# Kernel optimization log

Hardware: AMD Instinct MI355X
Metric: run time of the kernel (lower is better)

The kernel has to match this reference:

```python
import jax, jax.numpy as jnp
import numpy as np

B, C, H, W = 4, 64, 256, 256
HEADS = 8
EPS = 1e-12  # torch F.normalize eps


def _conv(x, w, groups=1, pad='VALID'):
    # x: [B,C,H,W], w: [O, I/groups, kh, kw]
    return jax.lax.conv_general_dilated(
        x, w, window_strides=(1, 1), padding=pad,
        feature_group_count=groups,
        dimension_numbers=('NCHW', 'OIHW', 'NCHW'))


def setup_inputs() -> dict:
    key = jax.random.key(0)
    ks = jax.random.split(key, 8)
    s = 0.02
    return {
        'input1': jax.random.normal(ks[0], (B, C, H, W), jnp.float32),
        'input2': jax.random.normal(ks[1], (B, C, H, W), jnp.float32),
        'q_w': jax.random.normal(ks[2], (C, C, 1, 1), jnp.float32) * s,
        'q_dw_w': jax.random.normal(ks[3], (C, 1, 3, 3), jnp.float32) * s,
        'kv_w': jax.random.normal(ks[4], (2 * C, C, 1, 1), jnp.float32) * s,
        'kv_dw_w': jax.random.normal(ks[5], (2 * C, 1, 3, 3), jnp.float32) * s,
        'proj_w': jax.random.normal(ks[6], (C, C, 1, 1), jnp.float32) * s,
        'temperature': jnp.ones((HEADS, 1, 1), jnp.float32),
    }


def reference(input1, input2, q_w, q_dw_w, kv_w, kv_dw_w, proj_w, temperature):
    b, c, h, w = input1.shape
    hd = c // HEADS  # per-head channels

    q = _conv(_conv(input1, q_w), q_dw_w, groups=c, pad=[(1, 1), (1, 1)])
    kv = _conv(_conv(input2, kv_w), kv_dw_w, groups=2 * c, pad=[(1, 1), (1, 1)])
    k, v = jnp.split(kv, 2, axis=1)

    # b (head c) h w -> b head c (h w)
    def to_heads(t):
        return t.reshape(b, HEADS, hd, h * w)

    q, k, v = to_heads(q), to_heads(k), to_heads(v)

    # L2-normalize over the large hw axis (torch F.normalize semantics)
    q = q / jnp.maximum(jnp.linalg.norm(q, axis=-1, keepdims=True), EPS)
    k = k / jnp.maximum(jnp.linalg.norm(k, axis=-1, keepdims=True), EPS)

    # tiny [b, head, c', c'] channel-attention matrix, contracted over hw
    attn = jnp.einsum('bhcn,bhdn->bhcd', q, k) * temperature
    attn = jax.nn.softmax(attn, axis=-1)
    out = jnp.einsum('bhcd,bhdn->bhcn', attn, v)

    out = out.reshape(b, c, h, w)
    return _conv(out, proj_w)
```

## Files before the change

### kernel.cpp

```cpp
#include <hip/hip_runtime.h>


#define HWN 65536
typedef unsigned short u16;

__device__ __forceinline__ float bf2f(u16 u) {
    return __uint_as_float(((unsigned int)u) << 16);
}
__device__ __forceinline__ u16 f2bf(float f) {
    unsigned int x = __float_as_uint(f);
    x += 0x7FFFu + ((x >> 16) & 1u);
    return (u16)(x >> 16);
}

template<int OC, bool IN_BF16, bool OUT_BF16, bool W_OIC, bool W_PERB>
__global__ __launch_bounds__(256) void pw_gemm(const void* __restrict__ in_v,
                                               const float* __restrict__ w_g,
                                               void* __restrict__ out_v)
{
    constexpr int G = OC / 16;
    constexpr int T = 256 / G;
    constexpr int PXB = T * 4;
    constexpr int NCHUNK = HWN / PXB;
    __shared__ float wlds[64 * OC];

    const int tid = threadIdx.x;
    const int b = blockIdx.y;
    const float* wsrc = w_g + (W_PERB ? b * 64 * OC : 0);

    for (int idx = tid * 4; idx < 64 * OC; idx += 1024) {
        float4 wv = *reinterpret_cast<const float4*>(wsrc + idx);
        if (W_OIC) {
            int oc = idx >> 6, ic0 = idx & 63;
            wlds[(ic0 + 0) * OC + oc] = wv.x;
            wlds[(ic0 + 1) * OC + oc] = wv.y;
            wlds[(ic0 + 2) * OC + oc] = wv.z;
            wlds[(ic0 + 3) * OC + oc] = wv.w;
        } else {
            *reinterpret_cast<float4*>(&wlds[idx]) = wv;
        }
    }
    __syncthreads();

    const int og = tid / T, tl = tid % T;
    const int ocb = og * 16;
    const size_t inb = (size_t)b * 64 * HWN;

    for (int chunk = blockIdx.x; chunk < NCHUNK; chunk += gridDim.x) {
        const int p0 = chunk * PXB + tl * 4;
        float acc[16][4];
#pragma unroll
        for (int o = 0; o < 16; ++o) {
            acc[o][0] = 0.f; acc[o][1] = 0.f; acc[o][2] = 0.f; acc[o][3] = 0.f;
        }
#pragma unroll 4
        for (int ic = 0; ic < 64; ++ic) {
            float x0, x1, x2, x3;
            if (IN_BF16) {
                ushort4 u = *reinterpret_cast<const ushort4*>(
                    (const u16*)in_v + inb + (size_t)ic * HWN + p0);
                x0 = bf2f(u.x); x1 = bf2f(u.y); x2 = bf2f(u.z); x3 = bf2f(u.w);
            } else {
                float4 f = *reinterpret_cast<const float4*>(
                    (const float*)in_v + inb + (size_t)ic * HWN + p0);
                x0 = f.x; x1 = f.y; x2 = f.z; x3 = f.w;
            }
            const float* wr = &wlds[ic * OC + ocb];
#pragma unroll
            for (int o = 0; o < 16; ++o) {
                const float wv = wr[o];
                acc[o][0] = fmaf(wv, x0, acc[o][0]);
                acc[o][1] = fmaf(wv, x1, acc[o][1]);
                acc[o][2] = fmaf(wv, x2, acc[o][2]);
                acc[o][3] = fmaf(wv, x3, acc[o][3]);
            }
        }
#pragma unroll
        for (int o = 0; o < 16; ++o) {
            const size_t ob = ((size_t)b * OC + ocb + o) * HWN + p0;
            if (OUT_BF16) {
                ushort4 u;
                u.x = f2bf(acc[o][0]); u.y = f2bf(acc[o][1]);
                u.z = f2bf(acc[o][2]); u.w = f2bf(acc[o][3]);
                *reinterpret_cast<ushort4*>((u16*)out_v + ob) = u;
            } else {
                float4 f;
                f.x = acc[o][0]; f.y = acc[o][1]; f.z = acc[o][2]; f.w = acc[o][3];
                *reinterpret_cast<float4*>((float*)out_v + ob) = f;
            }
        }
    }
}

#define RPW 2

__global__ __launch_bounds__(256) void qk_dots(const u16* __restrict__ tq,
                                               const u16* __restrict__ tkv,
                                               const float* __restrict__ qdw,
                                               const float* __restrict__ kvdw,
                                               float* __restrict__ ssq_q,
                                               float* __restrict__ ssq_k,
                                               float* __restrict__ qkout)
{
    const int b = blockIdx.z, hd = blockIdx.y;
    const int lane = threadIdx.x & 63, wid = threadIdx.x >> 6;
    const int row0 = blockIdx.x * (4 * RPW) + wid * RPW;

    __shared__ float wq[72], wk[72];
    if (threadIdx.x < 72)       wq[threadIdx.x] = qdw[hd * 72 + threadIdx.x];
    else if (threadIdx.x < 144) wk[threadIdx.x - 72] = kvdw[hd * 72 + (threadIdx.x - 72)];
    __syncthreads();

    const u16* qb = tq  + (size_t)(b * 64  + hd * 8) * HWN;
    const u16* kb = tkv + (size_t)(b * 128 + hd * 8) * HWN;
    const int wo = lane * 4;

    float A[64];
#pragma unroll
    for (int i = 0; i < 64; ++i) A[i] = 0.f;
    float sq[8] = {0.f, 0.f, 0.f, 0.f, 0.f, 0.f, 0.f, 0.f};
    float sk[8] = {0.f, 0.f, 0.f, 0.f, 0.f, 0.f, 0.f, 0.f};

#define DW4(PBASE, C, WTAB, A0, A1, A2, A3)                                    \
    {                                                                          \
        A0 = 0.f; A1 = 0.f; A2 = 0.f; A3 = 0.f;                                \
        const u16* p_ = (PBASE) + (size_t)(C) * HWN;                           \
        _Pragma("unroll")                                                      \
        for (int j = 0; j < 3; ++j) {                                          \
            const int hh = h - 1 + j;                                          \
            if (hh >= 0 && hh <= 255) {                                        \
                ushort4 u_ = *reinterpret_cast<const ushort4*>(p_ + hh * 256 + wo); \
                float x0 = bf2f(u_.x), x1 = bf2f(u_.y);                        \
                float x2 = bf2f(u_.z), x3 = bf2f(u_.w);                        \
                float xm1 = __shfl_up(x3, 1);  if (lane == 0)  xm1 = 0.f;      \
                float x4  = __shfl_down(x0, 1); if (lane == 63) x4 = 0.f;      \
                const float wa = WTAB[(C) * 9 + j * 3 + 0];                    \
                const float wb = WTAB[(C) * 9 + j * 3 + 1];                    \
                const float wc = WTAB[(C) * 9 + j * 3 + 2];                    \
                A0 = fmaf(wa, xm1, A0); A0 = fmaf(wb, x0, A0); A0 = fmaf(wc, x1, A0); \
                A1 = fmaf(wa, x0,  A1); A1 = fmaf(wb, x1, A1); A1 = fmaf(wc, x2, A1); \
                A2 = fmaf(wa, x1,  A2); A2 = fmaf(wb, x2, A2); A2 = fmaf(wc, x3, A2); \
                A3 = fmaf(wa, x2,  A3); A3 = fmaf(wb, x3, A3); A3 = fmaf(wc, x4, A3); \
            }                                                                  \
        }                                                                      \
    }

    for (int r = 0; r < RPW; ++r) {
        const int h = row0 + r;
        float qv[8][4];
#pragma unroll
        for (int c = 0; c < 8; ++c) {
            float a0, a1, a2, a3;
            DW4(qb, c, wq, a0, a1, a2, a3);
            qv[c][0] = a0; qv[c][1] = a1; qv[c][2] = a2; qv[c][3] = a3;
            sq[c] = fmaf(a0, a0, sq[c]); sq[c] = fmaf(a1, a1, sq[c]);
            sq[c] = fmaf(a2, a2, sq[c]); sq[c] = fmaf(a3, a3, sq[c]);
        }
#pragma unroll
        for (int d = 0; d < 8; ++d) {
            float k0, k1, k2, k3;
            DW4(kb, d, wk, k0, k1, k2, k3);
            sk[d] = fmaf(k0, k0, sk[d]); sk[d] = fmaf(k1, k1, sk[d]);
            sk[d] = fmaf(k2, k2, sk[d]); sk[d] = fmaf(k3, k3, sk[d]);
#pragma unroll
            for (int c = 0; c < 8; ++c) {
                float a = A[c * 8 + d];
                a = fmaf(qv[c][0], k0, a); a = fmaf(qv[c][1], k1, a);
                a = fmaf(qv[c][2], k2, a); a = fmaf(qv[c][3], k3, a);
                A[c * 8 + d] = a;
            }
        }
    }

#define REDSTEP(B, arr)                                                        \
    {                                                                          \
        const bool hi_ = (lane & (B)) != 0;                                    \
        _Pragma("unroll")                                                      \
        for (int i = 0; i < (B); ++i) {                                        \
            float keep_ = hi_ ? arr[i + (B)] : arr[i];                         \
            float send_ = hi_ ? arr[i] : arr[i + (B)];                         \
            arr[i] = keep_ + __shfl_xor(send_, (B));                           \
        }                                                                      \
    }
    REDSTEP(32, A) REDSTEP(16, A) REDSTEP(8, A)
    REDSTEP(4, A)  REDSTEP(2, A)  REDSTEP(1, A)
    atomicAdd(qkout + (size_t)(b * 8 + hd) * 64 + lane, A[0]);

    float S[16];
#pragma unroll
    for (int c = 0; c < 8; ++c) { S[c] = sq[c]; S[8 + c] = sk[c]; }
    REDSTEP(8, S) REDSTEP(4, S) REDSTEP(2, S) REDSTEP(1, S)
    float s = S[0];
    s += __shfl_xor(s, 16);
    s += __shfl_xor(s, 32);
    if (lane < 16) {
        float* dst = (lane < 8) ? (ssq_q + b * 64 + hd * 8 + lane)
                                : (ssq_k + b * 64 + hd * 8 + lane - 8);
        atomicAdd(dst, s);
    }
#undef DW4
#undef REDSTEP
}

__global__ __launch_bounds__(256) void dw_v(const u16* __restrict__ tkv,
                                            const float* __restrict__ kvdw,
                                            u16* __restrict__ vout)
{
    const int qid = blockIdx.x * 256 + threadIdx.x;
    const int w0 = (qid & 63) * 4;
    const int h  = (qid >> 6) & 255;
    const int ch = (qid >> 14) & 63;
    const int b  = qid >> 20;

    const u16* p = tkv + (size_t)(b * 128 + 64 + ch) * HWN;
    const float* wd = kvdw + (64 + ch) * 9;

    float a0 = 0.f, a1 = 0.f, a2 = 0.f, a3 = 0.f;
    const float mL = (w0 > 0) ? 1.f : 0.f;
    const float mR = (w0 < 252) ? 1.f : 0.f;
    const int iL = (w0 > 0) ? w0 - 1 : 0;
    const int iR = (w0 < 252) ? w0 + 4 : 255;
#pragma unroll
    for (int j = 0; j < 3; ++j) {
        const int hh = h - 1 + j;
        if (hh < 0 || hh > 255) continue;
        const int rb = hh * 256;
        float xm1 = bf2f(p[rb + iL]) * mL;
        ushort4 mu = *reinterpret_cast<const ushort4*>(p + rb + w0);
        float x0 = bf2f(mu.x), x1 = bf2f(mu.y), x2 = bf2f(mu.z), x3 = bf2f(mu.w);
        float x4 = bf2f(p[rb + iR]) * mR;
        const float wa = wd[j*3+0], wb = wd[j*3+1], wc = wd[j*3+2];
        a0 = fmaf(wa, xm1, a0); a0 = fmaf(wb, x0, a0); a0 = fmaf(wc, x1, a0);
        a1 = fmaf(wa, x0,  a1); a1 = fmaf(wb, x1, a1); a1 = fmaf(wc, x2, a1);
        a2 = fmaf(wa, x1,  a2); a2 = fmaf(wb, x2, a2); a2 = fmaf(wc, x3, a2);
        a3 = fmaf(wa, x2,  a3); a3 = fmaf(wb, x3, a3); a3 = fmaf(wc, x4, a3);
    }
    ushort4 o;
    o.x = f2bf(a0); o.y = f2bf(a1); o.z = f2bf(a2); o.w = f2bf(a3);
    *reinterpret_cast<ushort4*>(vout + (size_t)(b * 64 + ch) * HWN + h * 256 + w0) = o;
}

__global__ __launch_bounds__(64) void build_m(const float* __restrict__ ssq_q,
                                              const float* __restrict__ ssq_k,
                                              const float* __restrict__ qk,
                                              const float* __restrict__ temp,
                                              const float* __restrict__ projw,
                                              float* __restrict__ Mt)
{
    const int b = blockIdx.x, t = threadIdx.x;
    __shared__ float attn[8][8][8];
    {
        const int hd = t >> 3, c = t & 7;
        const float nq = fmaxf(sqrtf(ssq_q[b * 64 + hd * 8 + c]), 1e-12f);
        float s[8];
        float mx = -1e30f;
#pragma unroll
        for (int d = 0; d < 8; ++d) {
            const float nk = fmaxf(sqrtf(ssq_k[b * 64 + hd * 8 + d]), 1e-12f);
            s[d] = qk[(size_t)((b*8 + hd)*8 + c) * 8 + d] / (nq * nk) * temp[hd];
            mx = fmaxf(mx, s[d]);
        }
        float sum = 0.f;
#pragma unroll
        for (int d = 0; d < 8; ++d) { s[d] = expf(s[d] - mx); sum += s[d]; }
        const float inv = 1.f / sum;
#pragma unroll
        for (int d = 0; d < 8; ++d) attn[hd][c][d] = s[d] * inv;
    }
    __syncthreads();
    for (int hh = 0; hh < 8; ++hh) {
        float p8[8];
#pragma unroll
        for (int cl = 0; cl < 8; ++cl) p8[cl] = projw[t * 64 + hh * 8 + cl];
#pragma unroll
        for (int d = 0; d < 8; ++d) {
            float a = 0.f;
#pragma unroll
            for (int cl = 0; cl < 8; ++cl) a = fmaf(p8[cl], attn[hh][cl][d], a);
            Mt[b * 4096 + (hh * 8 + d) * 64 + t] = a;
        }
    }
}

extern "C" void kernel_launch(void* const* d_in, const int* in_sizes, int n_in,
                              void* d_out, int out_size, void* d_ws, size_t ws_size,
                              hipStream_t stream)
{
    const float* input1  = (const float*)d_in[0];
    const float* input2  = (const float*)d_in[1];
    const float* q_w     = (const float*)d_in[2];
    const float* q_dw_w  = (const float*)d_in[3];
    const float* kv_w    = (const float*)d_in[4];
    const float* kv_dw_w = (const float*)d_in[5];
    const float* proj_w  = (const float*)d_in[6];
    const float* temp    = (const float*)d_in[7];
    float* out = (float*)d_out;

    char* ws = (char*)d_ws;
    u16* t_kv = (u16*)ws;
    u16* t_q  = (u16*)(ws + 67108864);
    u16* v    = t_q;
    float* accs  = (float*)(ws + 100663296);
    float* ssq_q = accs;
    float* ssq_k = accs + 256;
    float* qk    = accs + 512;
    float* Mt    = accs + 2560;
    if (ws_size < 100663296ull + (2560ull + 16384ull) * 4ull) return;

    hipMemsetAsync(accs, 0, 2560 * sizeof(float), stream);

    pw_gemm<64, false, true, true, false><<<dim3(256, 4), 256, 0, stream>>>(input1, q_w, t_q);
    pw_gemm<128, false, true, true, false><<<dim3(256, 4), 256, 0, stream>>>(input2, kv_w, t_kv);
    qk_dots<<<dim3(32, 8, 4), 256, 0, stream>>>(t_q, t_kv, q_dw_w, kv_dw_w, ssq_q, ssq_k, qk);
    dw_v<<<16384, 256, 0, stream>>>(t_kv, kv_dw_w, v);
    build_m<<<4, 64, 0, stream>>>(ssq_q, ssq_k, qk, temp, proj_w, Mt);
    pw_gemm<64, true, false, false, true><<<dim3(256, 4), 256, 0, stream>>>(v, Mt, out);
}
```

Baseline: 494.5 us.

## Restructure qk_dots to stage depthwise outputs in LDS and vectorize weight reads

qk_dots now has each wave run the 3x3 depthwise conv on four of the sixteen q/k channels over a strip of four rows. Input rows are reused across output rows in registers, and the results are written as bf16 to LDS. After a barrier, each wave computes two q rows of the 8x8 Gram matrix plus the squared norms from LDS, which removes the 64-register accumulator array and the redundant halo loads. The k sums of squares are computed by all four waves, so they are scaled by 0.25 before the atomic add. Separately, pw_gemm reads its 16 weights per input channel as four float4 LDS loads instead of scalar loads. The q/k values are now rounded to bf16 before the dot products, which slightly changes numerics.

```diff
diff --git a/kernel.cpp b/kernel.cpp
--- a/kernel.cpp
+++ b/kernel.cpp
@@ -65,10 +65,17 @@
                     (const float*)in_v + inb + (size_t)ic * HWN + p0);
                 x0 = f.x; x1 = f.y; x2 = f.z; x3 = f.w;
             }
-            const float* wr = &wlds[ic * OC + ocb];
+            const float4 w4a = *reinterpret_cast<const float4*>(&wlds[ic * OC + ocb + 0]);
+            const float4 w4b = *reinterpret_cast<const float4*>(&wlds[ic * OC + ocb + 4]);
+            const float4 w4c = *reinterpret_cast<const float4*>(&wlds[ic * OC + ocb + 8]);
+            const float4 w4d = *reinterpret_cast<const float4*>(&wlds[ic * OC + ocb + 12]);
+            const float wv16[16] = {w4a.x, w4a.y, w4a.z, w4a.w,
+                                    w4b.x, w4b.y, w4b.z, w4b.w,
+                                    w4c.x, w4c.y, w4c.z, w4c.w,
+                                    w4d.x, w4d.y, w4d.z, w4d.w};
 #pragma unroll
             for (int o = 0; o < 16; ++o) {
-                const float wv = wr[o];
+                const float wv = wv16[o];
                 acc[o][0] = fmaf(wv, x0, acc[o][0]);
                 acc[o][1] = fmaf(wv, x1, acc[o][1]);
                 acc[o][2] = fmaf(wv, x2, acc[o][2]);
@@ -92,7 +99,7 @@
     }
 }
 
-#define RPW 2
+#define STRIP 4
 
 __global__ __launch_bounds__(256) void qk_dots(const u16* __restrict__ tq,
                                                const u16* __restrict__ tkv,
@@ -104,71 +111,96 @@
 {
     const int b = blockIdx.z, hd = blockIdx.y;
     const int lane = threadIdx.x & 63, wid = threadIdx.x >> 6;
-    const int row0 = blockIdx.x * (4 * RPW) + wid * RPW;
-
-    __shared__ float wq[72], wk[72];
-    if (threadIdx.x < 72)       wq[threadIdx.x] = qdw[hd * 72 + threadIdx.x];
-    else if (threadIdx.x < 144) wk[threadIdx.x - 72] = kvdw[hd * 72 + (threadIdx.x - 72)];
+    const int r0 = blockIdx.x * STRIP;
+
+    __shared__ u16 qklds[16][STRIP * 256];
+    __shared__ float wlds[144];
+
+    if (threadIdx.x < 72)       wlds[threadIdx.x] = qdw[hd * 72 + threadIdx.x];
+    else if (threadIdx.x < 144) wlds[threadIdx.x] = kvdw[hd * 72 + (threadIdx.x - 72)];
     __syncthreads();
 
-    const u16* qb = tq  + (size_t)(b * 64  + hd * 8) * HWN;
-    const u16* kb = tkv + (size_t)(b * 128 + hd * 8) * HWN;
+    const u16* qbase = tq  + (size_t)(b * 64  + hd * 8) * HWN;
+    const u16* kbase = tkv + (size_t)(b * 128 + hd * 8) * HWN;
     const int wo = lane * 4;
 
-    float A[64];
-#pragma unroll
-    for (int i = 0; i < 64; ++i) A[i] = 0.f;
-    float sq[8] = {0.f, 0.f, 0.f, 0.f, 0.f, 0.f, 0.f, 0.f};
-    float sk[8] = {0.f, 0.f, 0.f, 0.f, 0.f, 0.f, 0.f, 0.f};
-
-#define DW4(PBASE, C, WTAB, A0, A1, A2, A3)                                    \
-    {                                                                          \
-        A0 = 0.f; A1 = 0.f; A2 = 0.f; A3 = 0.f;                                \
-        const u16* p_ = (PBASE) + (size_t)(C) * HWN;                           \
-        _Pragma("unroll")                                                      \
-        for (int j = 0; j < 3; ++j) {                                          \
-            const int hh = h - 1 + j;                                          \
-            if (hh >= 0 && hh <= 255) {                                        \
-                ushort4 u_ = *reinterpret_cast<const ushort4*>(p_ + hh * 256 + wo); \
-                float x0 = bf2f(u_.x), x1 = bf2f(u_.y);                        \
-                float x2 = bf2f(u_.z), x3 = bf2f(u_.w);                        \
-                float xm1 = __shfl_up(x3, 1);  if (lane == 0)  xm1 = 0.f;      \
-                float x4  = __shfl_down(x0, 1); if (lane == 63) x4 = 0.f;      \
-                const float wa = WTAB[(C) * 9 + j * 3 + 0];                    \
-                const float wb = WTAB[(C) * 9 + j * 3 + 1];                    \
-                const float wc = WTAB[(C) * 9 + j * 3 + 2];                    \
-                A0 = fmaf(wa, xm1, A0); A0 = fmaf(wb, x0, A0); A0 = fmaf(wc, x1, A0); \
-                A1 = fmaf(wa, x0,  A1); A1 = fmaf(wb, x1, A1); A1 = fmaf(wc, x2, A1); \
-                A2 = fmaf(wa, x1,  A2); A2 = fmaf(wb, x2, A2); A2 = fmaf(wc, x3, A2); \
-                A3 = fmaf(wa, x2,  A3); A3 = fmaf(wb, x3, A3); A3 = fmaf(wc, x4, A3); \
-            }                                                                  \
-        }                                                                      \
-    }
-
-    for (int r = 0; r < RPW; ++r) {
-        const int h = row0 + r;
-        float qv[8][4];
-#pragma unroll
-        for (int c = 0; c < 8; ++c) {
-            float a0, a1, a2, a3;
-            DW4(qb, c, wq, a0, a1, a2, a3);
-            qv[c][0] = a0; qv[c][1] = a1; qv[c][2] = a2; qv[c][3] = a3;
-            sq[c] = fmaf(a0, a0, sq[c]); sq[c] = fmaf(a1, a1, sq[c]);
-            sq[c] = fmaf(a2, a2, sq[c]); sq[c] = fmaf(a3, a3, sq[c]);
-        }
+#pragma unroll 1
+    for (int i = 0; i < 4; ++i) {
+        const int gc = wid * 4 + i;
+        const u16* src = (gc < 8) ? (qbase + (size_t)gc * HWN)
+                                  : (kbase + (size_t)(gc - 8) * HWN);
+        float wreg[9];
+#pragma unroll
+        for (int t = 0; t < 9; ++t) wreg[t] = wlds[gc * 9 + t];
+
+        float R[STRIP + 2][6];
+#pragma unroll
+        for (int jr = 0; jr < STRIP + 2; ++jr) {
+            const int hh = r0 - 1 + jr;
+            if (hh >= 0 && hh <= 255) {
+                ushort4 u = *reinterpret_cast<const ushort4*>(src + hh * 256 + wo);
+                float x0 = bf2f(u.x), x1 = bf2f(u.y), x2 = bf2f(u.z), x3 = bf2f(u.w);
+                float xm1 = __shfl_up(x3, 1);  if (lane == 0)  xm1 = 0.f;
+                float x4  = __shfl_down(x0, 1); if (lane == 63) x4 = 0.f;
+                R[jr][0] = xm1; R[jr][1] = x0; R[jr][2] = x1;
+                R[jr][3] = x2;  R[jr][4] = x3; R[jr][5] = x4;
+            } else {
+#pragma unroll
+                for (int t = 0; t < 6; ++t) R[jr][t] = 0.f;
+            }
+        }
+#pragma unroll
+        for (int o = 0; o < STRIP; ++o) {
+            float a0 = 0.f, a1 = 0.f, a2 = 0.f, a3 = 0.f;
+#pragma unroll
+            for (int t = 0; t < 3; ++t) {
+                const float wa = wreg[t * 3 + 0];
+                const float wb = wreg[t * 3 + 1];
+                const float wc = wreg[t * 3 + 2];
+                a0 = fmaf(wa, R[o + t][0], a0); a0 = fmaf(wb, R[o + t][1], a0); a0 = fmaf(wc, R[o + t][2], a0);
+                a1 = fmaf(wa, R[o + t][1], a1); a1 = fmaf(wb, R[o + t][2], a1); a1 = fmaf(wc, R[o + t][3], a1);
+                a2 = fmaf(wa, R[o + t][2], a2); a2 = fmaf(wb, R[o + t][3], a2); a2 = fmaf(wc, R[o + t][4], a2);
+                a3 = fmaf(wa, R[o + t][3], a3); a3 = fmaf(wb, R[o + t][4], a3); a3 = fmaf(wc, R[o + t][5], a3);
+            }
+            uint2 pk;
+            pk.x = (unsigned int)f2bf(a0) | ((unsigned int)f2bf(a1) << 16);
+            pk.y = (unsigned int)f2bf(a2) | ((unsigned int)f2bf(a3) << 16);
+            *reinterpret_cast<uint2*>(&qklds[gc][o * 256 + wo]) = pk;
+        }
+    }
+    __syncthreads();
+
+    const int c0 = wid * 2;
+    float acc[2][8];
+#pragma unroll
+    for (int d = 0; d < 8; ++d) { acc[0][d] = 0.f; acc[1][d] = 0.f; }
+    float sq0 = 0.f, sq1 = 0.f;
+    float skk[8] = {0.f, 0.f, 0.f, 0.f, 0.f, 0.f, 0.f, 0.f};
+
+#pragma unroll
+    for (int chk = 0; chk < STRIP; ++chk) {
+        const int p = chk * 256 + wo;
+        uint2 qu0 = *reinterpret_cast<const uint2*>(&qklds[c0 + 0][p]);
+        uint2 qu1 = *reinterpret_cast<const uint2*>(&qklds[c0 + 1][p]);
+        float q0a = __uint_as_float(qu0.x << 16), q0b = __uint_as_float(qu0.x & 0xffff0000u);
+        float q0c = __uint_as_float(qu0.y << 16), q0d = __uint_as_float(qu0.y & 0xffff0000u);
+        float q1a = __uint_as_float(qu1.x << 16), q1b = __uint_as_float(qu1.x & 0xffff0000u);
+        float q1c = __uint_as_float(qu1.y << 16), q1d = __uint_as_float(qu1.y & 0xffff0000u);
+        sq0 = fmaf(q0a, q0a, sq0); sq0 = fmaf(q0b, q0b, sq0);
+        sq0 = fmaf(q0c, q0c, sq0); sq0 = fmaf(q0d, q0d, sq0);
+        sq1 = fmaf(q1a, q1a, sq1); sq1 = fmaf(q1b, q1b, sq1);
+        sq1 = fmaf(q1c, q1c, sq1); sq1 = fmaf(q1d, q1d, sq1);
 #pragma unroll
         for (int d = 0; d < 8; ++d) {
-            float k0, k1, k2, k3;
-            DW4(kb, d, wk, k0, k1, k2, k3);
-            sk[d] = fmaf(k0, k0, sk[d]); sk[d] = fmaf(k1, k1, sk[d]);
-            sk[d] = fmaf(k2, k2, sk[d]); sk[d] = fmaf(k3, k3, sk[d]);
-#pragma unroll
-            for (int c = 0; c < 8; ++c) {
-                float a = A[c * 8 + d];
-                a = fmaf(qv[c][0], k0, a); a = fmaf(qv[c][1], k1, a);
-                a = fmaf(qv[c][2], k2, a); a = fmaf(qv[c][3], k3, a);
-                A[c * 8 + d] = a;
-            }
+            uint2 ku = *reinterpret_cast<const uint2*>(&qklds[8 + d][p]);
+            float ka = __uint_as_float(ku.x << 16), kb = __uint_as_float(ku.x & 0xffff0000u);
+            float kc = __uint_as_float(ku.y << 16), kd = __uint_as_float(ku.y & 0xffff0000u);
+            skk[d] = fmaf(ka, ka, skk[d]); skk[d] = fmaf(kb, kb, skk[d]);
+            skk[d] = fmaf(kc, kc, skk[d]); skk[d] = fmaf(kd, kd, skk[d]);
+            acc[0][d] = fmaf(q0a, ka, acc[0][d]); acc[0][d] = fmaf(q0b, kb, acc[0][d]);
+            acc[0][d] = fmaf(q0c, kc, acc[0][d]); acc[0][d] = fmaf(q0d, kd, acc[0][d]);
+            acc[1][d] = fmaf(q1a, ka, acc[1][d]); acc[1][d] = fmaf(q1b, kb, acc[1][d]);
+            acc[1][d] = fmaf(q1c, kc, acc[1][d]); acc[1][d] = fmaf(q1d, kd, acc[1][d]);
         }
     }
 
@@ -182,23 +214,37 @@
             arr[i] = keep_ + __shfl_xor(send_, (B));                           \
         }                                                                      \
     }
-    REDSTEP(32, A) REDSTEP(16, A) REDSTEP(8, A)
-    REDSTEP(4, A)  REDSTEP(2, A)  REDSTEP(1, A)
-    atomicAdd(qkout + (size_t)(b * 8 + hd) * 64 + lane, A[0]);
-
-    float S[16];
-#pragma unroll
-    for (int c = 0; c < 8; ++c) { S[c] = sq[c]; S[8 + c] = sk[c]; }
-    REDSTEP(8, S) REDSTEP(4, S) REDSTEP(2, S) REDSTEP(1, S)
-    float s = S[0];
-    s += __shfl_xor(s, 16);
-    s += __shfl_xor(s, 32);
-    if (lane < 16) {
-        float* dst = (lane < 8) ? (ssq_q + b * 64 + hd * 8 + lane)
-                                : (ssq_k + b * 64 + hd * 8 + lane - 8);
-        atomicAdd(dst, s);
-    }
-#undef DW4
+
+    float A16[16];
+#pragma unroll
+    for (int d = 0; d < 8; ++d) { A16[d] = acc[0][d]; A16[8 + d] = acc[1][d]; }
+    REDSTEP(8, A16) REDSTEP(4, A16) REDSTEP(2, A16) REDSTEP(1, A16)
+    {
+        float s = A16[0];
+        s += __shfl_xor(s, 16);
+        s += __shfl_xor(s, 32);
+        if (lane < 16) {
+            const int cc = c0 + (lane >> 3), dd = lane & 7;
+            atomicAdd(qkout + (size_t)(b * 8 + hd) * 64 + cc * 8 + dd, s);
+        }
+    }
+    float S16[16];
+    S16[0] = sq0; S16[1] = sq1;
+#pragma unroll
+    for (int d = 0; d < 8; ++d) S16[2 + d] = skk[d] * 0.25f;
+#pragma unroll
+    for (int t = 10; t < 16; ++t) S16[t] = 0.f;
+    REDSTEP(8, S16) REDSTEP(4, S16) REDSTEP(2, S16) REDSTEP(1, S16)
+    {
+        float s = S16[0];
+        s += __shfl_xor(s, 16);
+        s += __shfl_xor(s, 32);
+        if (lane < 10) {
+            float* dst = (lane < 2) ? (ssq_q + b * 64 + hd * 8 + c0 + lane)
+                                    : (ssq_k + b * 64 + hd * 8 + (lane - 2));
+            atomicAdd(dst, s);
+        }
+    }
 #undef REDSTEP
 }
 
@@ -311,7 +357,7 @@
 
     pw_gemm<64, false, true, true, false><<<dim3(256, 4), 256, 0, stream>>>(input1, q_w, t_q);
     pw_gemm<128, false, true, true, false><<<dim3(256, 4), 256, 0, stream>>>(input2, kv_w, t_kv);
-    qk_dots<<<dim3(32, 8, 4), 256, 0, stream>>>(t_q, t_kv, q_dw_w, kv_dw_w, ssq_q, ssq_k, qk);
+    qk_dots<<<dim3(256 / STRIP, 8, 4), 256, 0, stream>>>(t_q, t_kv, q_dw_w, kv_dw_w, ssq_q, ssq_k, qk);
     dw_v<<<16384, 256, 0, stream>>>(t_kv, kv_dw_w, v);
     build_m<<<4, 64, 0, stream>>>(ssq_q, ssq_k, qk, temp, proj_w, Mt);
     pw_gemm<64, true, false, false, true><<<dim3(256, 4), 256, 0, stream>>>(v, Mt, out);
```

New measurement: 410.4 us. -17.0%, faster.
